# Optimization experiments

Hardware: AMD Instinct MI355X
Metric: run time of the kernel (lower is better)

The kernel has to match this reference:

```python
import jax, jax.numpy as jnp
import numpy as np

EPS = 1e-5

def layernorm2d(x, w, b):
    # nn.LayerNorm([T, C]): normalize jointly over last two dims, affine shape [T, C]
    mu = jnp.mean(x, axis=(-2, -1), keepdims=True)
    var = jnp.mean(jnp.square(x - mu), axis=(-2, -1), keepdims=True)
    return (x - mu) * jax.lax.rsqrt(var + EPS) * w + b


def setup_inputs() -> dict:
    key = jax.random.key(0)
    ks = jax.random.split(key, 10)
    B, T, C = 64, 512, 512
    s = 0.02
    inputs = jax.random.normal(ks[0], (B, T, C), dtype=jnp.float32)
    ln1_w = jnp.ones((T, C), dtype=jnp.float32)
    ln1_b = jnp.zeros((T, C), dtype=jnp.float32)
    ln2_w = jnp.ones((T, C), dtype=jnp.float32)
    ln2_b = jnp.zeros((T, C), dtype=jnp.float32)
    # TriU: row i holds the Linear(i+1,1) weights for prefix 0..i -> lower-triangular [T,T]
    tri_M = jax.random.normal(ks[1], (T, T), dtype=jnp.float32) * s
    tri_b = jax.random.normal(ks[2], (T,), dtype=jnp.float32) * s
    d1_w = jax.random.normal(ks[3], (C, C), dtype=jnp.float32) * s  # dense_1: out = x @ d1_w.T + d1_b
    d1_b = jax.random.normal(ks[4], (C,), dtype=jnp.float32) * s
    d2_w = jax.random.normal(ks[5], (C, C), dtype=jnp.float32) * s
    d2_b = jax.random.normal(ks[6], (C,), dtype=jnp.float32) * s
    return {"inputs": inputs, "ln1_w": ln1_w, "ln1_b": ln1_b,
            "ln2_w": ln2_w, "ln2_b": ln2_b,
            "tri_M": tri_M, "tri_b": tri_b,
            "d1_w": d1_w, "d1_b": d1_b, "d2_w": d2_w, "d2_b": d2_b}


def reference(inputs, ln1_w, ln1_b, ln2_w, ln2_b, tri_M, tri_b, d1_w, d1_b, d2_w, d2_b):
    # x: [B, T, C]
    x = layernorm2d(inputs, ln1_w, ln1_b)
    # TriU time mixer: out[b,i,c] = sum_{j<=i} M[i,j] * x[b,j,c] + tri_b[i]
    M = jnp.tril(tri_M)
    x = jnp.einsum('it,btc->bic', M, x) + tri_b[None, :, None]
    x = layernorm2d(x + inputs, ln2_w, ln2_b)
    # channel mixer MLP (dropout = 0)
    h = jax.nn.gelu(jnp.einsum('btc,hc->bth', x, d1_w) + d1_b, approximate=False)
    y = jnp.einsum('bth,ch->btc', h, d2_w) + d2_b
    return x + y
```

## Files before the change

kernel.cpp:

```cpp
#include <hip/hip_runtime.h>
#include <hip/hip_bf16.h>
#include <math.h>


#define B_ 64
#define T_ 512
#define C_ 512
#define TC_ (T_ * C_)
static_assert(TC_ == 262144, "");

typedef __attribute__((ext_vector_type(8))) short bf16x8;
typedef __attribute__((ext_vector_type(4))) float f32x4;

__device__ __forceinline__ unsigned short f2bf(float f) {
  union { float f; unsigned u; } v; v.f = f;
  unsigned r = v.u + 0x7FFF + ((v.u >> 16) & 1);
  return (unsigned short)(r >> 16);
}
__device__ __forceinline__ float bf2f(unsigned short h) {
  union { unsigned u; float f; } v; v.u = ((unsigned)h) << 16; return v.f;
}

__device__ __forceinline__ size_t pidx(int row, int k) {
  return ((size_t)((row >> 4) * 16 + (k >> 5)) * 64 + ((k >> 3) & 3) * 16 + (row & 15)) * 8 + (k & 7);
}

__global__ __launch_bounds__(256) void conv_pack(
    const float* __restrict__ triM, const float* __restrict__ d1w,
    const float* __restrict__ d2w, unsigned short* __restrict__ Mb,
    unsigned short* __restrict__ W1b, unsigned short* __restrict__ W2b) {
  const int cid = blockIdx.x * 256 + threadIdx.x;
  const int i = cid >> 6, g = cid & 63;
  const int jb = g * 8;
  const size_t src = (size_t)i * 512 + jb;
  const size_t dst = ((size_t)((i >> 4) * 16 + (g >> 2)) * 64 + (g & 3) * 16 + (i & 15)) * 8;
  alignas(16) unsigned short o[8];
#pragma unroll
  for (int jj = 0; jj < 8; ++jj) o[jj] = (jb + jj <= i) ? f2bf(triM[src + jj]) : (unsigned short)0;
  *(uint4*)&Mb[dst] = *(const uint4*)o;
#pragma unroll
  for (int jj = 0; jj < 8; ++jj) o[jj] = f2bf(d1w[src + jj]);
  *(uint4*)&W1b[dst] = *(const uint4*)o;
#pragma unroll
  for (int jj = 0; jj < 8; ++jj) o[jj] = f2bf(d2w[src + jj]);
  *(uint4*)&W2b[dst] = *(const uint4*)o;
}

__global__ __launch_bounds__(256) void ln_stats(const float* __restrict__ x,
                                                float* __restrict__ red) {
  const int b = blockIdx.x;
  const int s = blockIdx.y;
  const float4* p = (const float4*)(x + (size_t)b * TC_) + (size_t)s * 4096;
  float s1 = 0.f, s2 = 0.f;
  for (int i = threadIdx.x; i < 4096; i += 256) {
    float4 v = p[i];
    s1 += v.x + v.y + v.z + v.w;
    s2 += v.x * v.x + v.y * v.y + v.z * v.z + v.w * v.w;
  }
#pragma unroll
  for (int o = 32; o; o >>= 1) { s1 += __shfl_down(s1, o, 64); s2 += __shfl_down(s2, o, 64); }
  __shared__ float sm[8];
  const int w = threadIdx.x >> 6, lane = threadIdx.x & 63;
  if (lane == 0) { sm[w * 2] = s1; sm[w * 2 + 1] = s2; }
  __syncthreads();
  if (threadIdx.x == 0) {
    float a = 0.f, c = 0.f;
    for (int i = 0; i < 4; ++i) { a += sm[2 * i]; c += sm[2 * i + 1]; }
    atomicAdd(&red[b * 2], a);
    atomicAdd(&red[b * 2 + 1], c);
  }
}

__global__ __launch_bounds__(256) void ln1_norm_t(
    const float* __restrict__ x, const float* __restrict__ w,
    const float* __restrict__ bvec, const float* __restrict__ red1,
    unsigned short* __restrict__ XnTp) {
  __shared__ unsigned short tile[64][65];
  const int b = blockIdx.z;
  const int t0 = blockIdx.y * 64;
  const int c0 = blockIdx.x * 64;
  const float mu = red1[b * 2] * (1.f / TC_);
  const float rstd = rsqrtf(red1[b * 2 + 1] * (1.f / TC_) - mu * mu + 1e-5f);
  const int tid = threadIdx.x;
  const int r = tid >> 4;
  const int cg = (tid & 15) * 4;
#pragma unroll
  for (int rr = 0; rr < 4; ++rr) {
    const int t = t0 + rr * 16 + r;
    const float4 xv = *(const float4*)&x[((size_t)b * T_ + t) * C_ + c0 + cg];
    const float4 wv = *(const float4*)&w[(size_t)t * C_ + c0 + cg];
    const float4 bv = *(const float4*)&bvec[(size_t)t * C_ + c0 + cg];
    tile[rr * 16 + r][cg + 0] = f2bf((xv.x - mu) * rstd * wv.x + bv.x);
    tile[rr * 16 + r][cg + 1] = f2bf((xv.y - mu) * rstd * wv.y + bv.y);
    tile[rr * 16 + r][cg + 2] = f2bf((xv.z - mu) * rstd * wv.z + bv.z);
    tile[rr * 16 + r][cg + 3] = f2bf((xv.w - mu) * rstd * wv.w + bv.w);
  }
  __syncthreads();
  const int cl = tid >> 2;
  const int tg = (tid & 3) * 16;
  alignas(16) unsigned short tmp[16];
#pragma unroll
  for (int j = 0; j < 16; ++j) tmp[j] = tile[tg + j][cl];
  const int c = c0 + cl;
  const int tb = t0 + tg;
  const size_t chunk0 = (size_t)((c >> 4) * 16 + (tb >> 5)) * 64 +
                        ((tb >> 3) & 3) * 16 + (c & 15);
  unsigned short* o = XnTp + (size_t)b * TC_;
  *(uint4*)&o[chunk0 * 8]        = *(const uint4*)&tmp[0];
  *(uint4*)&o[(chunk0 + 16) * 8] = *(const uint4*)&tmp[8];
}

__device__ __forceinline__ void gemm_direct_packed(
    const unsigned short* __restrict__ Ab, const unsigned short* __restrict__ Bb,
    int ktiles, f32x4 acc[4][4]) {
  const unsigned short* ap[4];
  const unsigned short* bp[4];
#pragma unroll
  for (int r = 0; r < 4; ++r) ap[r] = Ab + (size_t)r * 8192;
#pragma unroll
  for (int c = 0; c < 4; ++c) bp[c] = Bb + (size_t)c * 8192;
  bf16x8 a[2][4], b[2][4];
#pragma unroll
  for (int r = 0; r < 4; ++r) a[0][r] = *(const bf16x8*)(ap[r]);
#pragma unroll
  for (int c = 0; c < 4; ++c) b[0][c] = *(const bf16x8*)(bp[c]);
  for (int kt = 0; kt < ktiles; kt += 2) {
    const int k1 = ((kt + 1) & 15) * 512;
    const int k2 = ((kt + 2) & 15) * 512;
#pragma unroll
    for (int r = 0; r < 4; ++r) a[1][r] = *(const bf16x8*)(ap[r] + k1);
#pragma unroll
    for (int c = 0; c < 4; ++c) b[1][c] = *(const bf16x8*)(bp[c] + k1);
#pragma unroll
    for (int r = 0; r < 4; ++r)
#pragma unroll
      for (int c = 0; c < 4; ++c)
        acc[r][c] = __builtin_amdgcn_mfma_f32_16x16x32_bf16(a[0][r], b[0][c], acc[r][c], 0, 0, 0);
#pragma unroll
    for (int r = 0; r < 4; ++r) a[0][r] = *(const bf16x8*)(ap[r] + k2);
#pragma unroll
    for (int c = 0; c < 4; ++c) b[0][c] = *(const bf16x8*)(bp[c] + k2);
#pragma unroll
    for (int r = 0; r < 4; ++r)
#pragma unroll
      for (int c = 0; c < 4; ++c)
        acc[r][c] = __builtin_amdgcn_mfma_f32_16x16x32_bf16(a[1][r], b[1][c], acc[r][c], 0, 0, 0);
  }
}

__global__ __launch_bounds__(256) void gemm_mixer(
    const unsigned short* __restrict__ Mb, const unsigned short* __restrict__ XnTp,
    const float* __restrict__ trib, const float* __restrict__ inp,
    unsigned short* __restrict__ Z, float* __restrict__ red2) {
  const int b = blockIdx.z;
  const int i0 = blockIdx.y * 128;
  const int c0 = blockIdx.x * 128;
  const int tid = threadIdx.x, lane = tid & 63, w = tid >> 6;
  const int wr = (w >> 1) * 64, wc = (w & 1) * 64, m16 = lane & 15, quad = lane >> 4;
  f32x4 acc[4][4];
#pragma unroll
  for (int r = 0; r < 4; ++r)
#pragma unroll
    for (int c = 0; c < 4; ++c) acc[r][c] = (f32x4){0.f, 0.f, 0.f, 0.f};
  gemm_direct_packed(Mb + (size_t)((i0 + wr) >> 4) * 8192 + lane * 8,
                     XnTp + (size_t)b * TC_ + (size_t)((c0 + wc) >> 4) * 8192 + lane * 8,
                     (i0 >> 5) + 4, acc);
  float s1 = 0.f, s2 = 0.f;
#pragma unroll
  for (int r = 0; r < 4; ++r) {
#pragma unroll
    for (int g = 0; g < 4; ++g) {
      const int i = i0 + wr + r * 16 + quad * 4 + g;
      const float tb = trib[i];
      const float* inrow = &inp[((size_t)b * T_ + i) * C_];
      unsigned short* zrow = &Z[((size_t)b * T_ + i) * C_];
#pragma unroll
      for (int c = 0; c < 4; ++c) {
        const int ch = c0 + wc + c * 16 + m16;
        const float v = acc[r][c][g] + tb + inrow[ch];
        zrow[ch] = f2bf(v);
        s1 += v; s2 += v * v;
      }
    }
  }
#pragma unroll
  for (int o = 32; o; o >>= 1) { s1 += __shfl_down(s1, o, 64); s2 += __shfl_down(s2, o, 64); }
  __shared__ float sm[8];
  if (lane == 0) { sm[w * 2] = s1; sm[w * 2 + 1] = s2; }
  __syncthreads();
  if (tid == 0) {
    float a = 0.f, c2 = 0.f;
    for (int i = 0; i < 4; ++i) { a += sm[2 * i]; c2 += sm[2 * i + 1]; }
    atomicAdd(&red2[b * 2], a);
    atomicAdd(&red2[b * 2 + 1], c2);
  }
}

__global__ __launch_bounds__(256) void ln2_norm(
    const unsigned short* __restrict__ Z, const float* __restrict__ red2,
    const float* __restrict__ w, const float* __restrict__ bvec,
    unsigned short* __restrict__ X2p) {
  const int rg = blockIdx.x;
  const int bb = rg >> 5;
  const float mu = red2[bb * 2] * (1.f / TC_);
  const float rstd = rsqrtf(red2[bb * 2 + 1] * (1.f / TC_) - mu * mu + 1e-5f);
  const int tid = threadIdx.x;
  const int wv = tid >> 6, cg = tid & 63;
#pragma unroll
  for (int it = 0; it < 4; ++it) {
    const int m = it * 4 + wv;
    const int row = rg * 16 + m;
    const int trow = row & 511;
    uint4 zp = *(const uint4*)&Z[(size_t)row * C_ + cg * 8];
    const unsigned short* zs = (const unsigned short*)&zp;
    alignas(16) float wvv[8], bvv[8];
    *(float4*)&wvv[0] = *(const float4*)&w[(size_t)trow * C_ + cg * 8];
    *(float4*)&wvv[4] = *(const float4*)&w[(size_t)trow * C_ + cg * 8 + 4];
    *(float4*)&bvv[0] = *(const float4*)&bvec[(size_t)trow * C_ + cg * 8];
    *(float4*)&bvv[4] = *(const float4*)&bvec[(size_t)trow * C_ + cg * 8 + 4];
    alignas(16) unsigned short o[8];
#pragma unroll
    for (int j = 0; j < 8; ++j)
      o[j] = f2bf((bf2f(zs[j]) - mu) * rstd * wvv[j] + bvv[j]);
    const size_t chunk = (size_t)rg * 1024 + (size_t)(cg >> 2) * 64 + (cg & 3) * 16 + m;
    *(uint4*)&X2p[chunk * 8] = *(const uint4*)o;
  }
}

__global__ __launch_bounds__(256) void gemm_d1(
    const unsigned short* __restrict__ X2p, const unsigned short* __restrict__ W1p,
    const float* __restrict__ d1b, unsigned short* __restrict__ Hp) {
  const int i0 = blockIdx.y * 128;
  const int n0 = blockIdx.x * 128;
  const int tid = threadIdx.x, lane = tid & 63, w = tid >> 6;
  const int wr = (w >> 1) * 64, wc = (w & 1) * 64, m16 = lane & 15, quad = lane >> 4;
  f32x4 acc[4][4];
#pragma unroll
  for (int r = 0; r < 4; ++r)
#pragma unroll
    for (int c = 0; c < 4; ++c) acc[r][c] = (f32x4){0.f, 0.f, 0.f, 0.f};
  gemm_direct_packed(X2p + (size_t)((i0 + wr) >> 4) * 8192 + lane * 8,
                     W1p + (size_t)((n0 + wc) >> 4) * 8192 + lane * 8, 16, acc);
#pragma unroll
  for (int r = 0; r < 4; ++r) {
#pragma unroll
    for (int g = 0; g < 4; ++g) {
      const int row = i0 + wr + r * 16 + quad * 4 + g;
#pragma unroll
      for (int c = 0; c < 4; ++c) {
        const int n = n0 + wc + c * 16 + m16;
        const float v = acc[r][c][g] + d1b[n];
        const float gl = 0.5f * v * (1.0f + erff(v * 0.70710678118654752f));
        Hp[pidx(row, n)] = f2bf(gl);
      }
    }
  }
}

__global__ __launch_bounds__(256) void gemm_d2(
    const unsigned short* __restrict__ Hp, const unsigned short* __restrict__ W2p,
    const float* __restrict__ d2b, const unsigned short* __restrict__ X2p,
    float* __restrict__ out) {
  const int i0 = blockIdx.y * 128;
  const int n0 = blockIdx.x * 128;
  const int tid = threadIdx.x, lane = tid & 63, w = tid >> 6;
  const int wr = (w >> 1) * 64, wc = (w & 1) * 64, m16 = lane & 15, quad = lane >> 4;
  f32x4 acc[4][4];
#pragma unroll
  for (int r = 0; r < 4; ++r)
#pragma unroll
    for (int c = 0; c < 4; ++c) acc[r][c] = (f32x4){0.f, 0.f, 0.f, 0.f};
  gemm_direct_packed(Hp + (size_t)((i0 + wr) >> 4) * 8192 + lane * 8,
                     W2p + (size_t)((n0 + wc) >> 4) * 8192 + lane * 8, 16, acc);
#pragma unroll
  for (int r = 0; r < 4; ++r) {
#pragma unroll
    for (int g = 0; g < 4; ++g) {
      const int row = i0 + wr + r * 16 + quad * 4 + g;
#pragma unroll
      for (int c = 0; c < 4; ++c) {
        const int n = n0 + wc + c * 16 + m16;
        out[(size_t)row * C_ + n] = acc[r][c][g] + d2b[n] + bf2f(X2p[pidx(row, n)]);
      }
    }
  }
}

extern "C" void kernel_launch(void* const* d_in, const int* in_sizes, int n_in,
                              void* d_out, int out_size, void* d_ws, size_t ws_size,
                              hipStream_t stream) {
  const float* inp  = (const float*)d_in[0];
  const float* ln1w = (const float*)d_in[1];
  const float* ln1b = (const float*)d_in[2];
  const float* ln2w = (const float*)d_in[3];
  const float* ln2b = (const float*)d_in[4];
  const float* triM = (const float*)d_in[5];
  const float* trib = (const float*)d_in[6];
  const float* d1w  = (const float*)d_in[7];
  const float* d1b  = (const float*)d_in[8];
  const float* d2w  = (const float*)d_in[9];
  const float* d2b  = (const float*)d_in[10];
  float* out = (float*)d_out;

  char* ws = (char*)d_ws;
  float* red1 = (float*)ws;
  float* red2 = (float*)(ws + 512);
  unsigned short* Mb  = (unsigned short*)(ws + 1024);
  unsigned short* W1b = Mb + TC_;
  unsigned short* W2b = W1b + TC_;
  unsigned short* XnT = W2b + TC_;
  unsigned short* Z   = XnT + (size_t)B_ * TC_;
  unsigned short* X2  = Z + (size_t)B_ * TC_;
  unsigned short* H   = X2 + (size_t)B_ * TC_;

  hipMemsetAsync(ws, 0, 1024, stream);
  conv_pack<<<128, 256, 0, stream>>>(triM, d1w, d2w, Mb, W1b, W2b);
  ln_stats<<<dim3(B_, 16), 256, 0, stream>>>(inp, red1);
  ln1_norm_t<<<dim3(8, 8, B_), 256, 0, stream>>>(inp, ln1w, ln1b, red1, XnT);
  gemm_mixer<<<dim3(4, 4, B_), 256, 0, stream>>>(Mb, XnT, trib, inp, Z, red2);
  ln2_norm<<<2048, 256, 0, stream>>>(Z, red2, ln2w, ln2b, X2);
  gemm_d1<<<dim3(4, 256), 256, 0, stream>>>(X2, W1b, d1b, H);
  gemm_d2<<<dim3(4, 256), 256, 0, stream>>>(H, W2b, d2b, X2, out);
}
```

Before: 282.7 us.

## Compute each 128x128 GEMM tile with a single wave instead of four

Each GEMM kernel (mixer, d1, d2) now runs one 64-lane wave per 128x128 output tile, holding an 8x8 grid of MFMA accumulators, instead of four waves each owning a 64x64 sub-tile. The aim is to raise operand reuse per wave: each A/B fragment loaded from global memory feeds eight MFMAs instead of four, which halves global load traffic per FLOP. The mixer's LDS cross-wave reduction is dropped in favour of direct per-wave atomics. In exchange, the 256 accumulator floats plus 32 bf16x8 operand registers per lane push VGPR/AGPR usage very high, so occupancy falls and the kernel may spill. Latency hiding now depends on only a few waves per CU.

After: 476.3 us. +68.4%, slower.

```diff
diff --git a/kernel.cpp b/kernel.cpp
--- a/kernel.cpp
+++ b/kernel.cpp
@@ -110,73 +110,67 @@
   *(uint4*)&o[(chunk0 + 16) * 8] = *(const uint4*)&tmp[8];
 }
 
-__device__ __forceinline__ void gemm_direct_packed(
+__device__ __forceinline__ void gemm_wave128(
     const unsigned short* __restrict__ Ab, const unsigned short* __restrict__ Bb,
-    int ktiles, f32x4 acc[4][4]) {
-  const unsigned short* ap[4];
-  const unsigned short* bp[4];
-#pragma unroll
-  for (int r = 0; r < 4; ++r) ap[r] = Ab + (size_t)r * 8192;
-#pragma unroll
-  for (int c = 0; c < 4; ++c) bp[c] = Bb + (size_t)c * 8192;
-  bf16x8 a[2][4], b[2][4];
-#pragma unroll
-  for (int r = 0; r < 4; ++r) a[0][r] = *(const bf16x8*)(ap[r]);
-#pragma unroll
-  for (int c = 0; c < 4; ++c) b[0][c] = *(const bf16x8*)(bp[c]);
+    int ktiles, f32x4 acc[8][8]) {
+  bf16x8 a[2][8], b[2][8];
+#pragma unroll
+  for (int r = 0; r < 8; ++r) a[0][r] = *(const bf16x8*)(Ab + (size_t)r * 8192);
+#pragma unroll
+  for (int c = 0; c < 8; ++c) b[0][c] = *(const bf16x8*)(Bb + (size_t)c * 8192);
   for (int kt = 0; kt < ktiles; kt += 2) {
     const int k1 = ((kt + 1) & 15) * 512;
     const int k2 = ((kt + 2) & 15) * 512;
 #pragma unroll
-    for (int r = 0; r < 4; ++r) a[1][r] = *(const bf16x8*)(ap[r] + k1);
-#pragma unroll
-    for (int c = 0; c < 4; ++c) b[1][c] = *(const bf16x8*)(bp[c] + k1);
-#pragma unroll
-    for (int r = 0; r < 4; ++r)
-#pragma unroll
-      for (int c = 0; c < 4; ++c)
+    for (int r = 0; r < 8; ++r) a[1][r] = *(const bf16x8*)(Ab + (size_t)r * 8192 + k1);
+#pragma unroll
+    for (int c = 0; c < 8; ++c) b[1][c] = *(const bf16x8*)(Bb + (size_t)c * 8192 + k1);
+#pragma unroll
+    for (int r = 0; r < 8; ++r)
+#pragma unroll
+      for (int c = 0; c < 8; ++c)
         acc[r][c] = __builtin_amdgcn_mfma_f32_16x16x32_bf16(a[0][r], b[0][c], acc[r][c], 0, 0, 0);
 #pragma unroll
-    for (int r = 0; r < 4; ++r) a[0][r] = *(const bf16x8*)(ap[r] + k2);
-#pragma unroll
-    for (int c = 0; c < 4; ++c) b[0][c] = *(const bf16x8*)(bp[c] + k2);
-#pragma unroll
-    for (int r = 0; r < 4; ++r)
-#pragma unroll
-      for (int c = 0; c < 4; ++c)
+    for (int r = 0; r < 8; ++r) a[0][r] = *(const bf16x8*)(Ab + (size_t)r * 8192 + k2);
+#pragma unroll
+    for (int c = 0; c < 8; ++c) b[0][c] = *(const bf16x8*)(Bb + (size_t)c * 8192 + k2);
+#pragma unroll
+    for (int r = 0; r < 8; ++r)
+#pragma unroll
+      for (int c = 0; c < 8; ++c)
         acc[r][c] = __builtin_amdgcn_mfma_f32_16x16x32_bf16(a[1][r], b[1][c], acc[r][c], 0, 0, 0);
   }
 }
 
-__global__ __launch_bounds__(256) void gemm_mixer(
+__global__ __launch_bounds__(64) void gemm_mixer(
     const unsigned short* __restrict__ Mb, const unsigned short* __restrict__ XnTp,
     const float* __restrict__ trib, const float* __restrict__ inp,
     unsigned short* __restrict__ Z, float* __restrict__ red2) {
   const int b = blockIdx.z;
   const int i0 = blockIdx.y * 128;
   const int c0 = blockIdx.x * 128;
-  const int tid = threadIdx.x, lane = tid & 63, w = tid >> 6;
-  const int wr = (w >> 1) * 64, wc = (w & 1) * 64, m16 = lane & 15, quad = lane >> 4;
-  f32x4 acc[4][4];
-#pragma unroll
-  for (int r = 0; r < 4; ++r)
-#pragma unroll
-    for (int c = 0; c < 4; ++c) acc[r][c] = (f32x4){0.f, 0.f, 0.f, 0.f};
-  gemm_direct_packed(Mb + (size_t)((i0 + wr) >> 4) * 8192 + lane * 8,
-                     XnTp + (size_t)b * TC_ + (size_t)((c0 + wc) >> 4) * 8192 + lane * 8,
-                     (i0 >> 5) + 4, acc);
+  const int lane = threadIdx.x;
+  const int m16 = lane & 15, quad = lane >> 4;
+  f32x4 acc[8][8];
+#pragma unroll
+  for (int r = 0; r < 8; ++r)
+#pragma unroll
+    for (int c = 0; c < 8; ++c) acc[r][c] = (f32x4){0.f, 0.f, 0.f, 0.f};
+  gemm_wave128(Mb + (size_t)(i0 >> 4) * 8192 + lane * 8,
+               XnTp + (size_t)b * TC_ + (size_t)(c0 >> 4) * 8192 + lane * 8,
+               (i0 >> 5) + 4, acc);
   float s1 = 0.f, s2 = 0.f;
 #pragma unroll
-  for (int r = 0; r < 4; ++r) {
+  for (int r = 0; r < 8; ++r) {
 #pragma unroll
     for (int g = 0; g < 4; ++g) {
-      const int i = i0 + wr + r * 16 + quad * 4 + g;
+      const int i = i0 + r * 16 + quad * 4 + g;
       const float tb = trib[i];
       const float* inrow = &inp[((size_t)b * T_ + i) * C_];
       unsigned short* zrow = &Z[((size_t)b * T_ + i) * C_];
 #pragma unroll
-      for (int c = 0; c < 4; ++c) {
-        const int ch = c0 + wc + c * 16 + m16;
+      for (int c = 0; c < 8; ++c) {
+        const int ch = c0 + c * 16 + m16;
         const float v = acc[r][c][g] + tb + inrow[ch];
         zrow[ch] = f2bf(v);
         s1 += v; s2 += v * v;
@@ -185,14 +179,9 @@
   }
 #pragma unroll
   for (int o = 32; o; o >>= 1) { s1 += __shfl_down(s1, o, 64); s2 += __shfl_down(s2, o, 64); }
-  __shared__ float sm[8];
-  if (lane == 0) { sm[w * 2] = s1; sm[w * 2 + 1] = s2; }
-  __syncthreads();
-  if (tid == 0) {
-    float a = 0.f, c2 = 0.f;
-    for (int i = 0; i < 4; ++i) { a += sm[2 * i]; c2 += sm[2 * i + 1]; }
-    atomicAdd(&red2[b * 2], a);
-    atomicAdd(&red2[b * 2 + 1], c2);
+  if (lane == 0) {
+    atomicAdd(&red2[b * 2], s1);
+    atomicAdd(&red2[b * 2 + 1], s2);
   }
 }
 
@@ -227,28 +216,28 @@
   }
 }
 
-__global__ __launch_bounds__(256) void gemm_d1(
+__global__ __launch_bounds__(64) void gemm_d1(
     const unsigned short* __restrict__ X2p, const unsigned short* __restrict__ W1p,
     const float* __restrict__ d1b, unsigned short* __restrict__ Hp) {
   const int i0 = blockIdx.y * 128;
   const int n0 = blockIdx.x * 128;
-  const int tid = threadIdx.x, lane = tid & 63, w = tid >> 6;
-  const int wr = (w >> 1) * 64, wc = (w & 1) * 64, m16 = lane & 15, quad = lane >> 4;
-  f32x4 acc[4][4];
-#pragma unroll
-  for (int r = 0; r < 4; ++r)
-#pragma unroll
-    for (int c = 0; c < 4; ++c) acc[r][c] = (f32x4){0.f, 0.f, 0.f, 0.f};
-  gemm_direct_packed(X2p + (size_t)((i0 + wr) >> 4) * 8192 + lane * 8,
-                     W1p + (size_t)((n0 + wc) >> 4) * 8192 + lane * 8, 16, acc);
-#pragma unroll
-  for (int r = 0; r < 4; ++r) {
+  const int lane = threadIdx.x;
+  const int m16 = lane & 15, quad = lane >> 4;
+  f32x4 acc[8][8];
+#pragma unroll
+  for (int r = 0; r < 8; ++r)
+#pragma unroll
+    for (int c = 0; c < 8; ++c) acc[r][c] = (f32x4){0.f, 0.f, 0.f, 0.f};
+  gemm_wave128(X2p + (size_t)(i0 >> 4) * 8192 + lane * 8,
+               W1p + (size_t)(n0 >> 4) * 8192 + lane * 8, 16, acc);
+#pragma unroll
+  for (int r = 0; r < 8; ++r) {
 #pragma unroll
     for (int g = 0; g < 4; ++g) {
-      const int row = i0 + wr + r * 16 + quad * 4 + g;
-#pragma unroll
-      for (int c = 0; c < 4; ++c) {
-        const int n = n0 + wc + c * 16 + m16;
+      const int row = i0 + r * 16 + quad * 4 + g;
+#pragma unroll
+      for (int c = 0; c < 8; ++c) {
+        const int n = n0 + c * 16 + m16;
         const float v = acc[r][c][g] + d1b[n];
         const float gl = 0.5f * v * (1.0f + erff(v * 0.70710678118654752f));
         Hp[pidx(row, n)] = f2bf(gl);
@@ -257,29 +246,29 @@
   }
 }
 
-__global__ __launch_bounds__(256) void gemm_d2(
+__global__ __launch_bounds__(64) void gemm_d2(
     const unsigned short* __restrict__ Hp, const unsigned short* __restrict__ W2p,
     const float* __restrict__ d2b, const unsigned short* __restrict__ X2p,
     float* __restrict__ out) {
   const int i0 = blockIdx.y * 128;
   const int n0 = blockIdx.x * 128;
-  const int tid = threadIdx.x, lane = tid & 63, w = tid >> 6;
-  const int wr = (w >> 1) * 64, wc = (w & 1) * 64, m16 = lane & 15, quad = lane >> 4;
-  f32x4 acc[4][4];
-#pragma unroll
-  for (int r = 0; r < 4; ++r)
-#pragma unroll
-    for (int c = 0; c < 4; ++c) acc[r][c] = (f32x4){0.f, 0.f, 0.f, 0.f};
-  gemm_direct_packed(Hp + (size_t)((i0 + wr) >> 4) * 8192 + lane * 8,
-                     W2p + (size_t)((n0 + wc) >> 4) * 8192 + lane * 8, 16, acc);
-#pragma unroll
-  for (int r = 0; r < 4; ++r) {
+  const int lane = threadIdx.x;
+  const int m16 = lane & 15, quad = lane >> 4;
+  f32x4 acc[8][8];
+#pragma unroll
+  for (int r = 0; r < 8; ++r)
+#pragma unroll
+    for (int c = 0; c < 8; ++c) acc[r][c] = (f32x4){0.f, 0.f, 0.f, 0.f};
+  gemm_wave128(Hp + (size_t)(i0 >> 4) * 8192 + lane * 8,
+               W2p + (size_t)(n0 >> 4) * 8192 + lane * 8, 16, acc);
+#pragma unroll
+  for (int r = 0; r < 8; ++r) {
 #pragma unroll
     for (int g = 0; g < 4; ++g) {
-      const int row = i0 + wr + r * 16 + quad * 4 + g;
-#pragma unroll
-      for (int c = 0; c < 4; ++c) {
-        const int n = n0 + wc + c * 16 + m16;
+      const int row = i0 + r * 16 + quad * 4 + g;
+#pragma unroll
+      for (int c = 0; c < 8; ++c) {
+        const int n = n0 + c * 16 + m16;
         out[(size_t)row * C_ + n] = acc[r][c][g] + d2b[n] + bf2f(X2p[pidx(row, n)]);
       }
     }
@@ -317,8 +306,8 @@
   conv_pack<<<128, 256, 0, stream>>>(triM, d1w, d2w, Mb, W1b, W2b);
   ln_stats<<<dim3(B_, 16), 256, 0, stream>>>(inp, red1);
   ln1_norm_t<<<dim3(8, 8, B_), 256, 0, stream>>>(inp, ln1w, ln1b, red1, XnT);
-  gemm_mixer<<<dim3(4, 4, B_), 256, 0, stream>>>(Mb, XnT, trib, inp, Z, red2);
+  gemm_mixer<<<dim3(4, 4, B_), 64, 0, stream>>>(Mb, XnT, trib, inp, Z, red2);
   ln2_norm<<<2048, 256, 0, stream>>>(Z, red2, ln2w, ln2b, X2);
-  gemm_d1<<<dim3(4, 256), 256, 0, stream>>>(X2, W1b, d1b, H);
-  gemm_d2<<<dim3(4, 256), 256, 0, stream>>>(H, W2b, d2b, X2, out);
-}
+  gemm_d1<<<dim3(4, 256), 64, 0, stream>>>(X2, W1b, d1b, H);
+  gemm_d2<<<dim3(4, 256), 64, 0, stream>>>(H, W2b, d2b, X2, out);
+}
```
